# Kernel optimization log

Measured on AMD Instinct MI355X. Metric: run time of the kernel, lower is better.

The kernel has to match this reference:

```python
import jax, jax.numpy as jnp
import numpy as np

EPS_BN = 1e-5
EPS_LN = 1e-5

def _bn(x, gamma, beta, ch_axis):
    # training-mode BatchNorm: batch stats over all axes except ch_axis (biased var)
    axes = tuple(i for i in range(x.ndim) if i != ch_axis)
    mean = x.mean(axes, keepdims=True)
    var = x.var(axes, keepdims=True)
    shp = [1] * x.ndim; shp[ch_axis] = -1
    return (x - mean) / jnp.sqrt(var + EPS_BN) * gamma.reshape(shp) + beta.reshape(shp)

def _ln(x, gamma, beta):
    mean = x.mean(-1, keepdims=True)
    var = x.var(-1, keepdims=True)
    return (x - mean) / jnp.sqrt(var + EPS_LN) * gamma + beta

def _spline(x, knots, cps):
    # x: (B,S); knots, cps: (K,). Single-pass bucketize + gather + lerp,
    # equivalent to the torch per-interval masked loop (boundary points take
    # the right interval's t=0 value, identical result).
    K = knots.shape[0]
    xn = (x - jnp.min(x)) / (jnp.max(x) - jnp.min(x) + 1e-6)
    idx = jnp.clip(jnp.searchsorted(knots, xn, side='right') - 1, 0, K - 2)
    k0, k1 = knots[idx], knots[idx + 1]
    t = (xn - k0) / (k1 - k0)
    val = (1.0 - t) * cps[idx] + t * cps[idx + 1]
    in_range = (xn >= knots[0]) & (xn <= knots[-1])
    return jnp.where(in_range, val, 0.0)

def _mha(x, in_w, in_b, out_w, out_b, H):
    # torch nn.MultiheadAttention with batch_first=False: dim0 is the sequence.
    L, N, D = x.shape
    hd = D // H
    qkv = x @ in_w.T + in_b                       # (L,N,3D)
    q, k, v = jnp.split(qkv, 3, axis=-1)
    q = q.reshape(L, N, H, hd) * (1.0 / np.sqrt(hd))
    k = k.reshape(L, N, H, hd)
    v = v.reshape(L, N, H, hd)
    scores = jnp.einsum('lnhd,mnhd->nhlm', q, k)  # (N,H,L,L)
    attn = jax.nn.softmax(scores, axis=-1)
    out = jnp.einsum('nhlm,mnhd->lnhd', attn, v).reshape(L, N, D)
    return out @ out_w.T + out_b

def setup_inputs() -> dict:
    B, S, D, F, K, H = 32, 1024, 512, 8, 32, 8
    key = jax.random.key(0)
    ks = jax.random.split(key, 12)
    s = 0.02
    inp = {
        'x': jax.random.normal(ks[0], (B, S, D), jnp.float32),
        'in_w': jax.random.normal(ks[1], (3 * D, D), jnp.float32) * s,
        'in_b': jnp.zeros((3 * D,), jnp.float32),
        'out_w': jax.random.normal(ks[2], (D, D), jnp.float32) * s,
        'out_b': jnp.zeros((D,), jnp.float32),
        'attn_g': jnp.ones((D,), jnp.float32),
        'attn_beta': jnp.zeros((D,), jnp.float32),
        'proj_w': jax.random.normal(ks[3], (F, D), jnp.float32) * s,
        'proj_b': jnp.zeros((F,), jnp.float32),
        'pn_g': jnp.ones((F,), jnp.float32),
        'pn_beta': jnp.zeros((F,), jnp.float32),
        'knots': jnp.tile(jnp.linspace(0.0, 1.0, K, dtype=jnp.float32)[None, :], (F, 1)),
        'cps': jax.random.normal(ks[4], (F, K), jnp.float32) / np.sqrt(K),
        'gate_w': jax.random.normal(ks[5], (2 * D, F), jnp.float32) * s,
        'gate_b': jnp.zeros((2 * D,), jnp.float32),
        'gbn_g': jnp.ones((S,), jnp.float32),   # BatchNorm1d(2*d_model) hits dim1 = seq (= 2*d_model)
        'gbn_beta': jnp.zeros((S,), jnp.float32),
        'ln_g': jnp.ones((D,), jnp.float32),
        'ln_beta': jnp.zeros((D,), jnp.float32),
        'outp_w': jax.random.normal(ks[6], (D, D), jnp.float32) * s,
        'outp_b': jnp.zeros((D,), jnp.float32),
        'on_g': jnp.ones((D,), jnp.float32),
        'on_beta': jnp.zeros((D,), jnp.float32),
    }
    return inp

def reference(x, in_w, in_b, out_w, out_b, attn_g, attn_beta, proj_w, proj_b,
              pn_g, pn_beta, knots, cps, gate_w, gate_b, gbn_g, gbn_beta,
              ln_g, ln_beta, outp_w, outp_b, on_g, on_beta):
    H = 8
    attn_out = _mha(x, in_w, in_b, out_w, out_b, H)          # (B,S,D)
    attn_out = _bn(attn_out, attn_g, attn_beta, 2)
    projected = x @ proj_w.T + proj_b                         # (B,S,F)
    projected = _bn(projected, pn_g, pn_beta, 2)
    transformed = jax.vmap(_spline, in_axes=(2, 0, 0), out_axes=2)(projected, knots, cps)  # (B,S,F)
    h = transformed @ gate_w.T + gate_b                       # (B,S,2D)
    h = _bn(h, gbn_g, gbn_beta, 1)                            # channel axis = seq (torch quirk)
    a, b = jnp.split(h, 2, axis=-1)
    glu = a * jax.nn.sigmoid(b)                               # (B,S,D)
    gated = _ln(glu, ln_g, ln_beta)
    out = gated @ outp_w.T + outp_b
    out = _bn(out, on_g, on_beta, 2)
    return x + attn_out + out
```

## Files before the change

kernel.cpp:

```cpp
#include <hip/hip_runtime.h>
#include <math.h>


#define SOFF_AMEAN 0
#define SOFF_ARSTD 512
#define SOFF_OMEAN 1024
#define SOFF_ORSTD 1536
#define SOFF_PMEAN 2048
#define SOFF_PRSTD 2056
#define SOFF_FMIN  2064
#define SOFF_FMAX  2072
#define SOFF_SMEAN 2080
#define SOFF_SRSTD 3104
#define SOFF_G1    4128
#define SOFF_GB    4136
#define SOFF_SGB   4144
#define SOFF_QGB   4145
#define SOFF_G2    4160
#define SOFF_PART  4224

typedef short bf16x8_t __attribute__((ext_vector_type(8)));
typedef float f32x4_t __attribute__((ext_vector_type(4)));
typedef unsigned short us8_t __attribute__((ext_vector_type(8)));

__device__ __forceinline__ unsigned short f2bf(float f) {
  unsigned u = __float_as_uint(f);
  u = (u + 0x7FFFu + ((u >> 16) & 1u)) >> 16;
  return (unsigned short)u;
}
__device__ __forceinline__ float b2f(unsigned short u) {
  return __uint_as_float(((unsigned)u) << 16);
}

#define BARR do { asm volatile("" ::: "memory"); __builtin_amdgcn_s_barrier(); asm volatile("" ::: "memory"); } while (0)

__global__ __launch_bounds__(256) void zero_kernel(float* __restrict__ p) {
  p[blockIdx.x * 256 + threadIdx.x] = 0.f;
}

__global__ __launch_bounds__(256) void cvt8_kernel(const float* __restrict__ src,
                                                   unsigned short* __restrict__ dst) {
  int i = blockIdx.x * 256 + threadIdx.x;
  float4 a = ((const float4*)src)[i * 2];
  float4 b = ((const float4*)src)[i * 2 + 1];
  us8_t o;
  o[0] = f2bf(a.x); o[1] = f2bf(a.y); o[2] = f2bf(a.z); o[3] = f2bf(a.w);
  o[4] = f2bf(b.x); o[5] = f2bf(b.y); o[6] = f2bf(b.z); o[7] = f2bf(b.w);
  *(us8_t*)(dst + (size_t)i * 8) = o;
}

template<int NT, bool OUT_BF16, bool STATS>
__global__ __launch_bounds__(512, 2) void gemm256_kernel(
    const unsigned short* __restrict__ A, const unsigned short* __restrict__ B,
    const float* __restrict__ bias, unsigned short* __restrict__ Cb,
    float* __restrict__ Cf, float* __restrict__ gstats, int N) {
  __shared__ unsigned short As[4][256 * 32];
  __shared__ unsigned short Bs[4][256 * 32];
  const int bi = blockIdx.x;
  const int xcd = bi & 7, jb = bi >> 3;
  const int m0 = (xcd * 16 + jb / NT) * 256;
  const int n0 = (jb % NT) * 256;
  const int t = threadIdx.x;
  const int w = t >> 6, lane = t & 63;
  const int wm = w >> 2, wn = w & 3;

  const unsigned short* gA = A + (size_t)(m0 + w * 16 + (lane >> 2)) * 512
                               + (((lane & 3) ^ ((lane >> 3) & 3)) * 8);
  const unsigned short* gB = B + (size_t)(n0 + w * 16 + (lane >> 2)) * 512
                               + (((lane & 3) ^ ((lane >> 3) & 3)) * 8);

  const int fr = lane & 15, g = lane >> 4;
  const int kf = (fr >> 1) & 3;

  f32x4_t acc[8][4];
#pragma unroll
  for (int i = 0; i < 8; ++i)
#pragma unroll
    for (int jj = 0; jj < 4; ++jj) acc[i][jj] = (f32x4_t){0.f, 0.f, 0.f, 0.f};

#define STAGE(KT) do { \
    __builtin_amdgcn_global_load_lds( \
        (const __attribute__((address_space(1))) void*)(gA + (KT) * 32), \
        (__attribute__((address_space(3))) void*)&As[(KT) & 3][(w * 16) * 32], 16, 0, 0); \
    __builtin_amdgcn_global_load_lds( \
        (const __attribute__((address_space(1))) void*)(gA + (KT) * 32 + 128 * 512), \
        (__attribute__((address_space(3))) void*)&As[(KT) & 3][(128 + w * 16) * 32], 16, 0, 0); \
    __builtin_amdgcn_global_load_lds( \
        (const __attribute__((address_space(1))) void*)(gB + (KT) * 32), \
        (__attribute__((address_space(3))) void*)&Bs[(KT) & 3][(w * 16) * 32], 16, 0, 0); \
    __builtin_amdgcn_global_load_lds( \
        (const __attribute__((address_space(1))) void*)(gB + (KT) * 32 + 128 * 512), \
        (__attribute__((address_space(3))) void*)&Bs[(KT) & 3][(128 + w * 16) * 32], 16, 0, 0); \
  } while (0)

  STAGE(0); STAGE(1); STAGE(2);
  asm volatile("s_waitcnt vmcnt(8)" ::: "memory");
  BARR;

#pragma unroll
  for (int kt = 0; kt < 16; ++kt) {
    if (kt < 13) STAGE(kt + 3);
    const unsigned short* asb = &As[kt & 3][0];
    const unsigned short* bsb = &Bs[kt & 3][0];
    bf16x8_t af[8], bf[4];
#pragma unroll
    for (int ni = 0; ni < 4; ++ni)
      bf[ni] = *(const bf16x8_t*)&bsb[(wn * 64 + ni * 16 + fr) * 32 + ((g ^ kf) * 8)];
#pragma unroll
    for (int mi = 0; mi < 8; ++mi)
      af[mi] = *(const bf16x8_t*)&asb[(wm * 128 + mi * 16 + fr) * 32 + ((g ^ kf) * 8)];
    __builtin_amdgcn_s_setprio(1);
#pragma unroll
    for (int mi = 0; mi < 8; ++mi)
#pragma unroll
      for (int ni = 0; ni < 4; ++ni)
        acc[mi][ni] = __builtin_amdgcn_mfma_f32_16x16x32_bf16(af[mi], bf[ni], acc[mi][ni], 0, 0, 0);
    __builtin_amdgcn_s_setprio(0);
    if (kt < 15) {
      if (kt <= 12)      asm volatile("s_waitcnt vmcnt(8)" ::: "memory");
      else if (kt == 13) asm volatile("s_waitcnt vmcnt(4)" ::: "memory");
      else               asm volatile("s_waitcnt vmcnt(0)" ::: "memory");
      BARR;
    }
  }
#undef STAGE

  const int cr = (lane >> 4) * 4, cc = lane & 15;
  float bv[4], lsum[4], lsq[4];
#pragma unroll
  for (int ni = 0; ni < 4; ++ni) {
    bv[ni] = bias[n0 + wn * 64 + ni * 16 + cc];
    lsum[ni] = 0.f; lsq[ni] = 0.f;
  }
#pragma unroll
  for (int mi = 0; mi < 8; ++mi) {
#pragma unroll
    for (int jj = 0; jj < 4; ++jj) {
      const size_t row = (size_t)(m0 + wm * 128 + mi * 16 + cr + jj);
#pragma unroll
      for (int ni = 0; ni < 4; ++ni) {
        int col = n0 + wn * 64 + ni * 16 + cc;
        float v = acc[mi][ni][jj] + bv[ni];
        if (OUT_BF16) Cb[row * N + col] = f2bf(v);
        else          Cf[row * N + col] = v;
        if (STATS) { lsum[ni] += v; lsq[ni] += v * v; }
      }
    }
  }
  if (STATS) {
#pragma unroll
    for (int ni = 0; ni < 4; ++ni) {
      float s = lsum[ni], q = lsq[ni];
      s += __shfl_xor(s, 16); s += __shfl_xor(s, 32);
      q += __shfl_xor(q, 16); q += __shfl_xor(q, 32);
      if (lane < 16) {
        int col = n0 + wn * 64 + ni * 16 + lane;
        atomicAdd(&gstats[col], s);
        atomicAdd(&gstats[512 + col], q);
      }
    }
  }
}

__global__ __launch_bounds__(512) void statsfin_kernel(const float* __restrict__ part,
                                                       float* __restrict__ stats, int off) {
  int t = threadIdx.x;
  float mean = part[t] / 32768.f;
  float var = part[512 + t] / 32768.f - mean * mean;
  stats[off + t] = mean;
  stats[off + 512 + t] = rsqrtf(var + 1e-5f);
}

__global__ __launch_bounds__(64) void attn3_kernel(const unsigned short* __restrict__ qkv,
                                                   unsigned short* __restrict__ ctxb) {
  const int n = blockIdx.x, h = blockIdx.y;
  const int lane = threadIdx.x;
  const int fr = lane & 15, g = lane >> 4;
  const int r = lane & 31, hi2 = lane >> 5;
  __shared__ unsigned short vt[64 * 32];

  const unsigned short* base = qkv + (size_t)n * 1536 + (size_t)h * 64;

#pragma unroll
  for (int i = 0; i < 4; ++i) {
    const int d0 = (i * 2 + hi2) * 8;
    union { us8_t v; unsigned u[4]; } ov;
    ov.v = *(const us8_t*)(base + (size_t)r * 1572864 + 1024 + d0);
#pragma unroll
    for (int w = 0; w < 4; ++w) {
      unsigned o = ov.u[w];
      unsigned pu = __shfl_xor(o, 1);
      unsigned val = (r & 1) ? ((pu >> 16) | (o & 0xFFFF0000u))
                             : ((o & 0xFFFFu) | (pu << 16));
      int dw = d0 + 2 * w + (r & 1);
      *(unsigned*)&vt[dw * 32 + (r >> 1) * 2] = val;
    }
  }

  bf16x8_t kfr[2][2], qfr[2][2];
#pragma unroll
  for (int mi = 0; mi < 2; ++mi)
#pragma unroll
    for (int s = 0; s < 2; ++s)
      kfr[mi][s] = *(const bf16x8_t*)(base + (size_t)(mi * 16 + fr) * 1572864 + 512 + s * 32 + g * 8);
#pragma unroll
  for (int li = 0; li < 2; ++li)
#pragma unroll
    for (int s = 0; s < 2; ++s)
      qfr[li][s] = *(const bf16x8_t*)(base + (size_t)(li * 16 + fr) * 1572864 + s * 32 + g * 8);

  f32x4_t st[2][2];
#pragma unroll
  for (int mi = 0; mi < 2; ++mi)
#pragma unroll
    for (int li = 0; li < 2; ++li) {
      st[mi][li] = (f32x4_t){0.f, 0.f, 0.f, 0.f};
#pragma unroll
      for (int s = 0; s < 2; ++s)
        st[mi][li] = __builtin_amdgcn_mfma_f32_16x16x32_bf16(kfr[mi][s], qfr[li][s], st[mi][li], 0, 0, 0);
    }

  __syncthreads();
  bf16x8_t vf[4];
#pragma unroll
  for (int dj = 0; dj < 4; ++dj)
    vf[dj] = *(const bf16x8_t*)&vt[(dj * 16 + fr) * 32 + g * 8];

  const bool pj = (g & 1) != 0, hb = (g >> 1) != 0;
  f32x4_t outacc[2][4];
#pragma unroll
  for (int li = 0; li < 2; ++li) {
    float mx = -3e38f;
#pragma unroll
    for (int mi = 0; mi < 2; ++mi)
#pragma unroll
      for (int rr = 0; rr < 4; ++rr) mx = fmaxf(mx, st[mi][li][rr]);
    mx = fmaxf(mx, __shfl_xor(mx, 16));
    mx = fmaxf(mx, __shfl_xor(mx, 32));
    float e[2][4]; float sm = 0.f;
#pragma unroll
    for (int mi = 0; mi < 2; ++mi)
#pragma unroll
      for (int rr = 0; rr < 4; ++rr) {
        float ev = __expf((st[mi][li][rr] - mx) * 0.125f);
        e[mi][rr] = ev; sm += ev;
      }
    sm += __shfl_xor(sm, 16);
    sm += __shfl_xor(sm, 32);
    float inv = 1.f / sm;
    unsigned ww00 = ((unsigned)f2bf(e[0][1] * inv) << 16) | f2bf(e[0][0] * inv);
    unsigned ww01 = ((unsigned)f2bf(e[0][3] * inv) << 16) | f2bf(e[0][2] * inv);
    unsigned ww10 = ((unsigned)f2bf(e[1][1] * inv) << 16) | f2bf(e[1][0] * inv);
    unsigned ww11 = ((unsigned)f2bf(e[1][3] * inv) << 16) | f2bf(e[1][2] * inv);
    unsigned pw00 = __shfl_xor(ww00, 16), pw01 = __shfl_xor(ww01, 16);
    unsigned pw10 = __shfl_xor(ww10, 16), pw11 = __shfl_xor(ww11, 16);
    unsigned s00 = pj ? (hb ? pw00 : pw10) : (hb ? ww00 : ww10);
    unsigned s01 = pj ? (hb ? pw01 : pw11) : (hb ? ww01 : ww11);
    unsigned s10 = pj ? (hb ? ww00 : ww10) : (hb ? pw00 : pw10);
    unsigned s11 = pj ? (hb ? ww01 : ww11) : (hb ? pw01 : pw11);
    unsigned sb00 = __shfl_xor(s00, 32), sb01 = __shfl_xor(s01, 32);
    unsigned sb10 = __shfl_xor(s10, 32), sb11 = __shfl_xor(s11, 32);
    unsigned k00 = pj ? (hb ? pw10 : pw00) : (hb ? ww10 : ww00);
    unsigned k01 = pj ? (hb ? pw11 : pw01) : (hb ? ww11 : ww01);
    unsigned k10 = pj ? (hb ? ww10 : ww00) : (hb ? pw10 : pw00);
    unsigned k11 = pj ? (hb ? ww11 : ww01) : (hb ? pw11 : pw01);
    const bool take = (pj != hb);
    union { unsigned u[4]; bf16x8_t v; } pa;
    pa.u[0] = take ? sb00 : k00;
    pa.u[1] = take ? sb01 : k01;
    pa.u[2] = take ? sb10 : k10;
    pa.u[3] = take ? sb11 : k11;
#pragma unroll
    for (int dj = 0; dj < 4; ++dj)
      outacc[li][dj] = __builtin_amdgcn_mfma_f32_16x16x32_bf16(
          pa.v, vf[dj], (f32x4_t){0.f, 0.f, 0.f, 0.f}, 0, 0, 0);
  }

#pragma unroll
  for (int li = 0; li < 2; ++li)
#pragma unroll
    for (int dj = 0; dj < 4; ++dj)
#pragma unroll
      for (int rr = 0; rr < 4; ++rr) {
        int l = li * 16 + g * 4 + rr;
        ctxb[((size_t)l * 1024 + n) * 512 + h * 64 + dj * 16 + fr] = f2bf(outacc[li][dj][rr]);
      }
}

__global__ __launch_bounds__(256) void proj_kernel(const float* __restrict__ x,
    const float* __restrict__ pw, const float* __restrict__ pb, float* __restrict__ p) {
  int blk = blockIdx.x, t = threadIdx.x;
  int r0 = blk * 64;
  __shared__ float xsp[64 * 33];
  __shared__ float pwc[8 * 33];
  int l = t >> 2, fg = t & 3;
  float acc0 = 0.f, acc1 = 0.f;
  for (int k0 = 0; k0 < 512; k0 += 32) {
    __syncthreads();
    for (int i = t; i < 2048; i += 256) { int ll = i >> 5, kk = i & 31; xsp[ll * 33 + kk] = x[(size_t)(r0 + ll) * 512 + k0 + kk]; }
    { int ff = t >> 5, kk = t & 31; pwc[ff * 33 + kk] = pw[ff * 512 + k0 + kk]; }
    __syncthreads();
#pragma unroll 8
    for (int kk = 0; kk < 32; ++kk) {
      float xv = xsp[l * 33 + kk];
      acc0 += xv * pwc[(fg * 2) * 33 + kk];
      acc1 += xv * pwc[(fg * 2 + 1) * 33 + kk];
    }
  }
  float2 o; o.x = acc0 + pb[fg * 2]; o.y = acc1 + pb[fg * 2 + 1];
  *(float2*)&p[(r0 + l) * 8 + fg * 2] = o;
}

__global__ __launch_bounds__(256) void projstats_kernel(const float* __restrict__ p,
                                                        float* __restrict__ part) {
  int t = threadIdx.x, blk = blockIdx.x;
  int f = t & 7;
  float s = 0.f, s2 = 0.f;
  for (int r = blk * 32 + (t >> 3); r < 32768; r += 2048) { float v = p[r * 8 + f]; s += v; s2 += v * v; }
  __shared__ float red[256], red2[256];
  red[t] = s; red2[t] = s2; __syncthreads();
  for (int off = 128; off >= 8; off >>= 1) { if (t < off) { red[t] += red[t + off]; red2[t] += red2[t + off]; } __syncthreads(); }
  if (t < 8) { part[blk * 16 + t] = red[t]; part[blk * 16 + 8 + t] = red2[t]; }
}
__global__ void projfin_kernel(const float* __restrict__ part, float* __restrict__ stats) {
  int t = threadIdx.x;
  if (t < 8) {
    float s = 0.f, s2 = 0.f;
    for (int b = 0; b < 64; ++b) { s += part[b * 16 + t]; s2 += part[b * 16 + 8 + t]; }
    float mean = s / 32768.f;
    float var = s2 / 32768.f - mean * mean;
    stats[SOFF_PMEAN + t] = mean;
    stats[SOFF_PRSTD + t] = rsqrtf(var + 1e-5f);
  }
}

__global__ __launch_bounds__(256) void bnminmax_kernel(float* __restrict__ p,
    const float* __restrict__ stats, const float* __restrict__ png,
    const float* __restrict__ pnb, float* __restrict__ part) {
  int t = threadIdx.x, blk = blockIdx.x;
  int i0 = blk * 256 + t;
  int f = i0 & 7;
  float k1 = stats[SOFF_PRSTD + f] * png[f];
  float k0 = pnb[f] - stats[SOFF_PMEAN + f] * k1;
  float mn = 3e38f, mx = -3e38f;
  for (int i = i0; i < 262144; i += 16384) {
    float v = p[i] * k1 + k0;
    p[i] = v;
    mn = fminf(mn, v); mx = fmaxf(mx, v);
  }
  __shared__ float rmn[256], rmx[256];
  rmn[t] = mn; rmx[t] = mx; __syncthreads();
  for (int off = 128; off >= 8; off >>= 1) {
    if (t < off) { rmn[t] = fminf(rmn[t], rmn[t + off]); rmx[t] = fmaxf(rmx[t], rmx[t + off]); }
    __syncthreads();
  }
  if (t < 8) { part[blk * 16 + t] = rmn[t]; part[blk * 16 + 8 + t] = rmx[t]; }
}
__global__ void minmaxfin_kernel(const float* __restrict__ part, float* __restrict__ stats) {
  int t = threadIdx.x;
  if (t < 8) {
    float mn = 3e38f, mx = -3e38f;
    for (int b = 0; b < 64; ++b) { mn = fminf(mn, part[b * 16 + t]); mx = fmaxf(mx, part[b * 16 + 8 + t]); }
    stats[SOFF_FMIN + t] = mn;
    stats[SOFF_FMAX + t] = mx;
  }
}

__global__ __launch_bounds__(256) void spline_kernel(float* __restrict__ p,
    const float* __restrict__ knots, const float* __restrict__ cps,
    const float* __restrict__ stats) {
  __shared__ float ksh[8 * 33], csh[8 * 33];
  int t = threadIdx.x;
  { int f = t >> 5, j = t & 31; ksh[f * 33 + j] = knots[t]; csh[f * 33 + j] = cps[t]; }
  __syncthreads();
  int i = blockIdx.x * 256 + t;
  int f = i & 7;
  float xv = p[i];
  float mn = stats[SOFF_FMIN + f], mx = stats[SOFF_FMAX + f];
  float xn = (xv - mn) / (mx - mn + 1e-6f);
  const float* kn = &ksh[f * 33];
  const float* cp = &csh[f * 33];
  int pcnt = 0;
#pragma unroll
  for (int j = 0; j < 32; ++j) pcnt += (kn[j] <= xn) ? 1 : 0;
  int idx = pcnt - 1;
  idx = idx < 0 ? 0 : (idx > 30 ? 30 : idx);
  float k0v = kn[idx], k1v = kn[idx + 1];
  float tt = (xn - k0v) / (k1v - k0v);
  float val = (1.f - tt) * cp[idx] + tt * cp[idx + 1];
  bool inr = (xn >= kn[0]) && (xn <= kn[31]);
  p[i] = inr ? val : 0.f;
}

__global__ __launch_bounds__(256) void gateprep_kernel(const float* __restrict__ gw,
    const float* __restrict__ gb, float* __restrict__ stats) {
  int b = blockIdx.x, t = threadIdx.x;
  __shared__ float red[256];
  float s = 0.f;
  if (b < 64) {
    int f1 = b >> 3, f2 = b & 7;
    for (int j = t; j < 1024; j += 256) s += gw[j * 8 + f1] * gw[j * 8 + f2];
  } else if (b < 72) {
    int f = b - 64;
    for (int j = t; j < 1024; j += 256) s += gw[j * 8 + f];
  } else if (b < 80) {
    int f = b - 72;
    for (int j = t; j < 1024; j += 256) s += gb[j] * gw[j * 8 + f];
  } else if (b == 80) {
    for (int j = t; j < 1024; j += 256) s += gb[j];
  } else {
    for (int j = t; j < 1024; j += 256) s += gb[j] * gb[j];
  }
  red[t] = s; __syncthreads();
  for (int off = 128; off > 0; off >>= 1) { if (t < off) red[t] += red[t + off]; __syncthreads(); }
  if (t == 0) {
    float v = red[0];
    if (b < 64) stats[SOFF_G2 + b] = v;
    else if (b < 72) stats[SOFF_G1 + (b - 64)] = v;
    else if (b < 80) stats[SOFF_GB + (b - 72)] = v;
    else if (b == 80) stats[SOFF_SGB] = v;
    else stats[SOFF_QGB] = v;
  }
}

__global__ __launch_bounds__(256) void sstats_kernel(const float* __restrict__ tbuf,
                                                     float* __restrict__ stats) {
  int s = blockIdx.x, t = threadIdx.x;
  __shared__ float tv[256];
  __shared__ float red[256];
  __shared__ float T1[8];
  __shared__ float Ms[64];
  int b = t >> 3, f = t & 7;
  tv[t] = tbuf[(b * 1024 + s) * 8 + f];
  __syncthreads();
  red[t] = tv[t]; __syncthreads();
  for (int off = 128; off >= 8; off >>= 1) { if (t < off) red[t] += red[t + off]; __syncthreads(); }
  if (t < 8) T1[t] = red[t];
  if (t < 64) {
    int f1 = t >> 3, f2 = t & 7; float sM = 0.f;
    for (int bb = 0; bb < 32; ++bb) sM += tv[bb * 8 + f1] * tv[bb * 8 + f2];
    Ms[t] = sM;
  }
  __syncthreads();
  if (t == 0) {
    float sh = 0.f, s2 = 0.f;
    for (int ff = 0; ff < 8; ++ff) {
      sh += stats[SOFF_G1 + ff] * T1[ff];
      s2 += 2.f * stats[SOFF_GB + ff] * T1[ff];
    }
    sh += 32.f * stats[SOFF_SGB];
    for (int i = 0; i < 64; ++i) s2 += Ms[i] * stats[SOFF_G2 + i];
    s2 += 32.f * stats[SOFF_QGB];
    float mean = sh / 32768.f;
    float var = s2 / 32768.f - mean * mean;
    stats[SOFF_SMEAN + s] = mean;
    stats[SOFF_SRSTD + s] = rsqrtf(var + 1e-5f);
  }
}

__global__ __launch_bounds__(256) void gluln_kernel(const float* __restrict__ tbuf,
    const float* __restrict__ gw, const float* __restrict__ gb,
    const float* __restrict__ stats, const float* __restrict__ gbng,
    const float* __restrict__ gbnb, const float* __restrict__ lng,
    const float* __restrict__ lnb, unsigned short* __restrict__ gatedb) {
  const int t = threadIdx.x, wave = t >> 6, lane = t & 63;
  for (int rr = 0; rr < 4; ++rr) {
    const int r = blockIdx.x * 16 + wave * 4 + rr;
    const int s = r & 1023;
    float4 tA = *(const float4*)&tbuf[r * 8];
    float4 tB = *(const float4*)&tbuf[r * 8 + 4];
    float smean = stats[SOFF_SMEAN + s], srstd = stats[SOFF_SRSTD + s];
    float k1 = srstd * gbng[s];
    float k0 = gbnb[s] - smean * k1;
    float g[8];
    float sum = 0.f, sq = 0.f;
#pragma unroll
    for (int i = 0; i < 8; ++i) {
      int c = i * 64 + lane;
      float4 wa0 = *(const float4*)&gw[c * 8];
      float4 wa1 = *(const float4*)&gw[c * 8 + 4];
      float4 wb0 = *(const float4*)&gw[(c + 512) * 8];
      float4 wb1 = *(const float4*)&gw[(c + 512) * 8 + 4];
      float ha = tA.x * wa0.x + tA.y * wa0.y + tA.z * wa0.z + tA.w * wa0.w
               + tB.x * wa1.x + tB.y * wa1.y + tB.z * wa1.z + tB.w * wa1.w + gb[c];
      float hb = tA.x * wb0.x + tA.y * wb0.y + tA.z * wb0.z + tA.w * wb0.w
               + tB.x * wb1.x + tB.y * wb1.y + tB.z * wb1.z + tB.w * wb1.w + gb[c + 512];
      ha = ha * k1 + k0;
      hb = hb * k1 + k0;
      float gv = ha / (1.f + __expf(-hb));
      g[i] = gv; sum += gv; sq += gv * gv;
    }
#pragma unroll
    for (int m = 32; m >= 1; m >>= 1) { sum += __shfl_xor(sum, m); sq += __shfl_xor(sq, m); }
    float mean = sum * (1.f / 512.f);
    float rstd = rsqrtf(sq * (1.f / 512.f) - mean * mean + 1e-5f);
#pragma unroll
    for (int i = 0; i < 8; ++i) {
      int c = i * 64 + lane;
      gatedb[(size_t)r * 512 + c] = f2bf((g[i] - mean) * rstd * lng[c] + lnb[c]);
    }
  }
}

__global__ __launch_bounds__(256) void final_kernel(const float* __restrict__ x,
    const float* __restrict__ attn, const float* __restrict__ outl,
    const float* __restrict__ stats, const float* __restrict__ ag,
    const float* __restrict__ ab, const float* __restrict__ og,
    const float* __restrict__ ob, float* __restrict__ y) {
  int idx = blockIdx.x * 256 + threadIdx.x;
  int c4 = (idx & 127) * 4;
  float4 xv = ((const float4*)x)[idx];
  float4 av = ((const float4*)attn)[idx];
  float4 ov = ((const float4*)outl)[idx];
  float4 am = *(const float4*)&stats[SOFF_AMEAN + c4];
  float4 ar = *(const float4*)&stats[SOFF_ARSTD + c4];
  float4 om = *(const float4*)&stats[SOFF_OMEAN + c4];
  float4 orr = *(const float4*)&stats[SOFF_ORSTD + c4];
  float4 g1 = *(const float4*)&ag[c4];
  float4 b1 = *(const float4*)&ab[c4];
  float4 g2 = *(const float4*)&og[c4];
  float4 b2 = *(const float4*)&ob[c4];
  float4 o;
  o.x = xv.x + (av.x - am.x) * ar.x * g1.x + b1.x + (ov.x - om.x) * orr.x * g2.x + b2.x;
  o.y = xv.y + (av.y - am.y) * ar.y * g1.y + b1.y + (ov.y - om.y) * orr.y * g2.y + b2.y;
  o.z = xv.z + (av.z - am.z) * ar.z * g1.z + b1.z + (ov.z - om.z) * orr.z * g2.z + b2.z;
  o.w = xv.w + (av.w - am.w) * ar.w * g1.w + b1.w + (ov.w - om.w) * orr.w * g2.w + b2.w;
  ((float4*)y)[idx] = o;
}

extern "C" void kernel_launch(void* const* d_in, const int* in_sizes, int n_in,
                              void* d_out, int out_size, void* d_ws, size_t ws_size,
                              hipStream_t stream) {
  (void)in_sizes; (void)n_in; (void)out_size; (void)ws_size;
  const float* x        = (const float*)d_in[0];
  const float* in_w     = (const float*)d_in[1];
  const float* in_b     = (const float*)d_in[2];
  const float* out_w    = (const float*)d_in[3];
  const float* out_b    = (const float*)d_in[4];
  const float* attn_g   = (const float*)d_in[5];
  const float* attn_bt  = (const float*)d_in[6];
  const float* proj_w   = (const float*)d_in[7];
  const float* proj_b   = (const float*)d_in[8];
  const float* pn_g     = (const float*)d_in[9];
  const float* pn_bt    = (const float*)d_in[10];
  const float* knots    = (const float*)d_in[11];
  const float* cps      = (const float*)d_in[12];
  const float* gate_w   = (const float*)d_in[13];
  const float* gate_b   = (const float*)d_in[14];
  const float* gbn_g    = (const float*)d_in[15];
  const float* gbn_bt   = (const float*)d_in[16];
  const float* ln_g     = (const float*)d_in[17];
  const float* ln_bt    = (const float*)d_in[18];
  const float* outp_w   = (const float*)d_in[19];
  const float* outp_b   = (const float*)d_in[20];
  const float* on_g     = (const float*)d_in[21];
  const float* on_bt    = (const float*)d_in[22];

  float* out = (float*)d_out;
  unsigned short* xb      = (unsigned short*)d_ws;
  unsigned short* qkv_b   = xb + 16777216;
  unsigned short* ctx_b   = qkv_b + 50331648;
  unsigned short* wqkv_b  = ctx_b + 16777216;
  unsigned short* wout_b  = wqkv_b + 786432;
  unsigned short* woutp_b = wout_b + 262144;
  float* proj  = (float*)(woutp_b + 262144);
  float* stats = proj + 262144;
  float* part  = stats + SOFF_PART;
  float* partA  = part;
  float* partO  = part + 1024;
  float* partP  = part + 2048;
  float* partMM = part + 3072;
  float* attnf = (float*)qkv_b;
  unsigned short* gated_b = xb;

  zero_kernel<<<dim3(8), dim3(256), 0, stream>>>(part);
  cvt8_kernel<<<dim3(8192), dim3(256), 0, stream>>>(x, xb);
  cvt8_kernel<<<dim3(384), dim3(256), 0, stream>>>(in_w, wqkv_b);
  cvt8_kernel<<<dim3(128), dim3(256), 0, stream>>>(out_w, wout_b);
  cvt8_kernel<<<dim3(128), dim3(256), 0, stream>>>(outp_w, woutp_b);
  gemm256_kernel<6, true, false><<<dim3(768), dim3(512), 0, stream>>>(
      xb, wqkv_b, in_b, qkv_b, nullptr, nullptr, 1536);
  attn3_kernel<<<dim3(1024, 8), dim3(64), 0, stream>>>(qkv_b, ctx_b);
  gemm256_kernel<2, false, true><<<dim3(256), dim3(512), 0, stream>>>(
      ctx_b, wout_b, out_b, nullptr, attnf, partA, 512);
  statsfin_kernel<<<dim3(1), dim3(512), 0, stream>>>(partA, stats, SOFF_AMEAN);
  proj_kernel<<<dim3(512), dim3(256), 0, stream>>>(x, proj_w, proj_b, proj);
  projstats_kernel<<<dim3(64), dim3(256), 0, stream>>>(proj, partP);
  projfin_kernel<<<dim3(1), dim3(64), 0, stream>>>(partP, stats);
  bnminmax_kernel<<<dim3(64), dim3(256), 0, stream>>>(proj, stats, pn_g, pn_bt, partMM);
  minmaxfin_kernel<<<dim3(1), dim3(64), 0, stream>>>(partMM, stats);
  spline_kernel<<<dim3(1024), dim3(256), 0, stream>>>(proj, knots, cps, stats);
  gateprep_kernel<<<dim3(88), dim3(256), 0, stream>>>(gate_w, gate_b, stats);
  sstats_kernel<<<dim3(1024), dim3(256), 0, stream>>>(proj, stats);
  gluln_kernel<<<dim3(2048), dim3(256), 0, stream>>>(proj, gate_w, gate_b, stats,
                                                     gbn_g, gbn_bt, ln_g, ln_bt, gated_b);
  gemm256_kernel<2, false, true><<<dim3(256), dim3(512), 0, stream>>>(
      gated_b, woutp_b, outp_b, nullptr, out, partO, 512);
  statsfin_kernel<<<dim3(1), dim3(512), 0, stream>>>(partO, stats, SOFF_OMEAN);
  final_kernel<<<dim3(16384), dim3(256), 0, stream>>>(x, attnf, out, stats,
                                                      attn_g, attn_bt, on_g, on_bt, out);
}
```

Baseline: 470.3 us.

## Restructure bf16 GEMM mainloop to 64-wide K tiles with double-buffered sub-phase pipelining

Switches the 256x256 GEMM from a 4-stage ring of 32-wide K tiles to a 2-buffer scheme with 64-wide K tiles. Each K tile is split into four sub-phases whose A/B global-to-LDS loads are interleaved with MFMA work, using a new XOR swizzle over 8 column groups. The aim is fewer barrier-separated iterations and finer overlap of loads with math at the same LDS footprint. In exchange there are two barriers per sub-phase and more complex vmcnt bookkeeping, where a wrong wait count would be a correctness hazard.

```diff
diff --git a/kernel.cpp b/kernel.cpp
--- a/kernel.cpp
+++ b/kernel.cpp
@@ -34,6 +34,10 @@
 
 #define BARR do { asm volatile("" ::: "memory"); __builtin_amdgcn_s_barrier(); asm volatile("" ::: "memory"); } while (0)
 
+#define GLL(gp, lp) __builtin_amdgcn_global_load_lds( \
+    (const __attribute__((address_space(1))) void*)(gp), \
+    (__attribute__((address_space(3))) void*)(lp), 16, 0, 0)
+
 __global__ __launch_bounds__(256) void zero_kernel(float* __restrict__ p) {
   p[blockIdx.x * 256 + threadIdx.x] = 0.f;
 }
@@ -54,8 +58,8 @@
     const unsigned short* __restrict__ A, const unsigned short* __restrict__ B,
     const float* __restrict__ bias, unsigned short* __restrict__ Cb,
     float* __restrict__ Cf, float* __restrict__ gstats, int N) {
-  __shared__ unsigned short As[4][256 * 32];
-  __shared__ unsigned short Bs[4][256 * 32];
+  __shared__ unsigned short As[2][256 * 64];
+  __shared__ unsigned short Bs[2][256 * 64];
   const int bi = blockIdx.x;
   const int xcd = bi & 7, jb = bi >> 3;
   const int m0 = (xcd * 16 + jb / NT) * 256;
@@ -64,13 +68,14 @@
   const int w = t >> 6, lane = t & 63;
   const int wm = w >> 2, wn = w & 3;
 
-  const unsigned short* gA = A + (size_t)(m0 + w * 16 + (lane >> 2)) * 512
-                               + (((lane & 3) ^ ((lane >> 3) & 3)) * 8);
-  const unsigned short* gB = B + (size_t)(n0 + w * 16 + (lane >> 2)) * 512
-                               + (((lane & 3) ^ ((lane >> 3) & 3)) * 8);
+  const int rs = w * 8 + (lane >> 3);
+  const int rbase = rs + ((rs >> 5) * 96);
+  const unsigned short* gA = A + (size_t)(m0 + rbase) * 512 + (((lane & 7) ^ (lane >> 3)) * 8);
+  const unsigned short* gB = B + (size_t)(n0 + rbase) * 512 + (((lane & 7) ^ (lane >> 3)) * 8);
+  const int abrow = w * 8 + ((w >> 2) * 96);
 
   const int fr = lane & 15, g = lane >> 4;
-  const int kf = (fr >> 1) & 3;
+  const int sw = fr & 7;
 
   f32x4_t acc[8][4];
 #pragma unroll
@@ -78,52 +83,74 @@
 #pragma unroll
     for (int jj = 0; jj < 4; ++jj) acc[i][jj] = (f32x4_t){0.f, 0.f, 0.f, 0.f};
 
-#define STAGE(KT) do { \
-    __builtin_amdgcn_global_load_lds( \
-        (const __attribute__((address_space(1))) void*)(gA + (KT) * 32), \
-        (__attribute__((address_space(3))) void*)&As[(KT) & 3][(w * 16) * 32], 16, 0, 0); \
-    __builtin_amdgcn_global_load_lds( \
-        (const __attribute__((address_space(1))) void*)(gA + (KT) * 32 + 128 * 512), \
-        (__attribute__((address_space(3))) void*)&As[(KT) & 3][(128 + w * 16) * 32], 16, 0, 0); \
-    __builtin_amdgcn_global_load_lds( \
-        (const __attribute__((address_space(1))) void*)(gB + (KT) * 32), \
-        (__attribute__((address_space(3))) void*)&Bs[(KT) & 3][(w * 16) * 32], 16, 0, 0); \
-    __builtin_amdgcn_global_load_lds( \
-        (const __attribute__((address_space(1))) void*)(gB + (KT) * 32 + 128 * 512), \
-        (__attribute__((address_space(3))) void*)&Bs[(KT) & 3][(128 + w * 16) * 32], 16, 0, 0); \
-  } while (0)
-
-  STAGE(0); STAGE(1); STAGE(2);
-  asm volatile("s_waitcnt vmcnt(8)" ::: "memory");
+#pragma unroll
+  for (int q = 0; q < 4; ++q)
+    GLL(gA + (size_t)(q * 32) * 512, &As[0][(q * 32 + abrow) * 64]);
+#pragma unroll
+  for (int q = 0; q < 4; ++q)
+    GLL(gB + (size_t)(q * 32) * 512, &Bs[0][(q * 32 + abrow) * 64]);
+#pragma unroll
+  for (int q = 0; q < 3; ++q)
+    GLL(gB + (size_t)(q * 32) * 512 + 64, &Bs[1][(q * 32 + abrow) * 64]);
+  asm volatile("s_waitcnt vmcnt(3)" ::: "memory");
   BARR;
 
 #pragma unroll
-  for (int kt = 0; kt < 16; ++kt) {
-    if (kt < 13) STAGE(kt + 3);
-    const unsigned short* asb = &As[kt & 3][0];
-    const unsigned short* bsb = &Bs[kt & 3][0];
-    bf16x8_t af[8], bf[4];
-#pragma unroll
-    for (int ni = 0; ni < 4; ++ni)
-      bf[ni] = *(const bf16x8_t*)&bsb[(wn * 64 + ni * 16 + fr) * 32 + ((g ^ kf) * 8)];
-#pragma unroll
-    for (int mi = 0; mi < 8; ++mi)
-      af[mi] = *(const bf16x8_t*)&asb[(wm * 128 + mi * 16 + fr) * 32 + ((g ^ kf) * 8)];
-    __builtin_amdgcn_s_setprio(1);
-#pragma unroll
-    for (int mi = 0; mi < 8; ++mi)
-#pragma unroll
-      for (int ni = 0; ni < 4; ++ni)
-        acc[mi][ni] = __builtin_amdgcn_mfma_f32_16x16x32_bf16(af[mi], bf[ni], acc[mi][ni], 0, 0, 0);
-    __builtin_amdgcn_s_setprio(0);
-    if (kt < 15) {
-      if (kt <= 12)      asm volatile("s_waitcnt vmcnt(8)" ::: "memory");
-      else if (kt == 13) asm volatile("s_waitcnt vmcnt(4)" ::: "memory");
-      else               asm volatile("s_waitcnt vmcnt(0)" ::: "memory");
+  for (int kt = 0; kt < 8; ++kt) {
+    const int d = kt & 1;
+    const unsigned short* asb = &As[d][0];
+    const unsigned short* bsb = &Bs[d][0];
+    bf16x8_t bfr[4][2];
+#pragma unroll
+    for (int q = 0; q < 4; ++q) {
+      const int gph = kt * 4 + q;
+      if (q == 0) {
+#pragma unroll
+        for (int ni = 0; ni < 4; ++ni)
+#pragma unroll
+          for (int ks = 0; ks < 2; ++ks)
+            bfr[ni][ks] = *(const bf16x8_t*)&bsb[(wn * 64 + ni * 16 + fr) * 64
+                                                 + (((ks * 4 + g) ^ sw) * 8)];
+      }
+      bf16x8_t af[2][2];
+#pragma unroll
+      for (int m2 = 0; m2 < 2; ++m2)
+#pragma unroll
+        for (int ks = 0; ks < 2; ++ks)
+          af[m2][ks] = *(const bf16x8_t*)&asb[(wm * 128 + (q * 2 + m2) * 16 + fr) * 64
+                                              + (((ks * 4 + g) ^ sw) * 8)];
+      if (kt < 7)
+        GLL(gA + (size_t)(q * 32) * 512 + (size_t)(kt + 1) * 64,
+            &As[d ^ 1][(q * 32 + abrow) * 64]);
+      if (q == 0) {
+        if (kt < 7)
+          GLL(gB + (size_t)(3 * 32) * 512 + (size_t)(kt + 1) * 64,
+              &Bs[d ^ 1][(3 * 32 + abrow) * 64]);
+      } else if (kt < 6) {
+        GLL(gB + (size_t)((q - 1) * 32) * 512 + (size_t)(kt + 2) * 64,
+            &Bs[d][((q - 1) * 32 + abrow) * 64]);
+      }
+      if (gph <= 24)      asm volatile("s_waitcnt vmcnt(6)" ::: "memory");
+      else if (gph == 25) asm volatile("s_waitcnt vmcnt(5)" ::: "memory");
+      else if (gph == 26) asm volatile("s_waitcnt vmcnt(4)" ::: "memory");
+      else if (gph == 27) asm volatile("s_waitcnt vmcnt(3)" ::: "memory");
+      else if (gph == 28) asm volatile("s_waitcnt vmcnt(2)" ::: "memory");
+      else if (gph == 29) asm volatile("s_waitcnt vmcnt(1)" ::: "memory");
+      else if (gph == 30) asm volatile("s_waitcnt vmcnt(0)" ::: "memory");
       BARR;
-    }
-  }
-#undef STAGE
+      __builtin_amdgcn_s_setprio(1);
+#pragma unroll
+      for (int ks = 0; ks < 2; ++ks)
+#pragma unroll
+        for (int m2 = 0; m2 < 2; ++m2)
+#pragma unroll
+          for (int ni = 0; ni < 4; ++ni)
+            acc[q * 2 + m2][ni] = __builtin_amdgcn_mfma_f32_16x16x32_bf16(
+                af[m2][ks], bfr[ni][ks], acc[q * 2 + m2][ni], 0, 0, 0);
+      __builtin_amdgcn_s_setprio(0);
+      BARR;
+    }
+  }
 
   const int cr = (lane >> 4) * 4, cc = lane & 15;
   float bv[4], lsum[4], lsq[4];
```

Result: slower. 489.6 us (+4.1%).
